# Kernel tuning notes

Measured on AMD Instinct MI355X. Metric: run time of the kernel, lower is better.

The kernel has to match this reference:

```python
import jax, jax.numpy as jnp
import numpy as np

S, B_BOX, N_CLASS = 7, 2, 20
L_COORD, L_NOOBJ = 5.0, 0.5
BATCH = 4096
C = 5 * B_BOX + N_CLASS  # 30


def setup_inputs() -> dict:
    key = jax.random.key(0)
    k1, k2, k3, k4 = jax.random.split(key, 4)
    # coords/w/h/classes strictly positive (sqrt is applied to raw values)
    y = jax.random.uniform(k1, (BATCH, S, S, C), minval=0.05, maxval=0.95, dtype=jnp.float32)
    # confidence channels must be exactly 0/1 (mask tests == 1)
    conf0 = jax.random.bernoulli(k3, 0.3, (BATCH, S, S)).astype(jnp.float32)
    conf1 = jax.random.bernoulli(k4, 0.3, (BATCH, S, S)).astype(jnp.float32)
    y = y.at[..., 0].set(conf0).at[..., 5].set(conf1)
    y_h = jax.random.uniform(k2, (BATCH, S, S, C), minval=0.05, maxval=0.95, dtype=jnp.float32)
    return {"y": y, "y_h": y_h}


def _loss(y, y_h):
    b_sz = y.shape[0]
    conf_idx = np.arange(B_BOX) * 5  # [0, 5]
    y_conf = y[..., conf_idx]        # [B,S,S,b]
    yh_conf = y_h[..., conf_idx]
    mf = (y_conf == 1.0).astype(y.dtype)  # obj mask per box, constant wrt grads
    dconf = (y_conf - yh_conf) ** 2
    loss_obj = jnp.sum(dconf * mf)
    loss_noobj = jnp.sum(dconf * (1.0 - mf))

    loss_coord = jnp.zeros((), y.dtype)
    loss_prob = jnp.zeros((), y.dtype)
    for k in range(B_BOX):  # static small loop over boxes
        mk = mf[..., k]  # [B,S,S]
        base = 5 * k
        dxy = (y[..., base + 1] - y_h[..., base + 1]) ** 2 \
            + (y[..., base + 2] - y_h[..., base + 2]) ** 2
        dwh = (jnp.sqrt(y[..., base + 3]) - jnp.sqrt(y_h[..., base + 3])) ** 2 \
            + (jnp.sqrt(y[..., base + 4]) - jnp.sqrt(y_h[..., base + 4])) ** 2
        loss_coord = loss_coord + jnp.sum((dxy + dwh) * mk)

        # prob term: slice from k*5+5 to end (faithful to original, for k=0 this
        # includes box-2's 5 entries), softmax over the masked batch dimension.
        tail = y[..., base + 5:]
        tail_h = y_h[..., base + 5:]
        mkb = mk[..., None]  # [B,S,S,1]
        neg = jnp.where(mkb > 0, tail_h, -jnp.inf)
        m = jnp.max(neg, axis=0)                       # [S,S,Ct]
        m_safe = jnp.where(jnp.isfinite(m), m, 0.0)    # guard empty columns
        p = jnp.exp(tail_h - m_safe) * mkb
        denom = jnp.sum(p, axis=0)
        sm = p / jnp.where(denom > 0, denom, 1.0)
        loss_prob = loss_prob + jnp.sum((tail - sm) ** 2 * mkb)

    loss = loss_obj + L_NOOBJ * loss_noobj + L_COORD * loss_coord + loss_prob
    return loss / b_sz


def reference(y, y_h):
    return _loss(y, y_h)
```

## Files before the change

kernel.cpp:

```cpp
#include <hip/hip_runtime.h>
#include <math.h>

#define CC 30
#define NBATCH 4096
#define NIJ 49
#define NPAIR 1225
#define PSTR 7352
#define F4TOT (PSTR / 4)
#define THREADS 512
#define SLABF4 1470
#define SLABF  5880


__global__ __launch_bounds__(THREADS)
void yolo_main(const float* __restrict__ y, const float* __restrict__ yh,
               float* __restrict__ scal, float* __restrict__ parts, int nwg)
{
    __shared__ __align__(16) float tY[2][SLABF];
    __shared__ __align__(16) float tH[2][SLABF];
    __shared__ float scr[4][8];

    const int tid = threadIdx.x;
    const int wg  = blockIdx.x;
    const int bpw = NBATCH / nwg;
    const int nslab = bpw >> 2;

    const int i0 = tid, i1 = tid + 512;
    const int i2r = tid + 1024;
    const int i2  = (i2r < SLABF4) ? i2r : (SLABF4 - 1);
    const bool w2 = (i2r < SLABF4);

    int  ijv[3], cv[3], pr[3];
    bool val[3];
    #pragma unroll
    for (int i = 0; i < 3; i++) {
        int p = tid + i * THREADS;
        val[i] = (p < NPAIR);
        pr[i]  = p;
        int pp = val[i] ? p : 0;
        ijv[i] = pp / 25;
        cv[i]  = 5 + pp % 25;
    }

    float D0[3] = {0,0,0}, B0[3] = {0,0,0}, C0[3] = {0,0,0};
    float D1[3] = {0,0,0}, B1[3] = {0,0,0}, C1[3] = {0,0,0};
    float obj = 0.f, noobj = 0.f, coord = 0.f, tt = 0.f;

    const float4* Yg = (const float4*)y;
    const float4* Hg = (const float4*)yh;

    {
        const size_t f4 = (size_t)((wg * bpw) >> 2) * SLABF4;
        float4 a0 = Yg[f4+i0], a1 = Yg[f4+i1], a2 = Yg[f4+i2];
        float4 b0 = Hg[f4+i0], b1 = Hg[f4+i1], b2 = Hg[f4+i2];
        float4* dY = (float4*)tY[0];
        float4* dH = (float4*)tH[0];
        dY[i0] = a0; dY[i1] = a1; if (w2) dY[i2] = a2;
        dH[i0] = b0; dH[i1] = b1; if (w2) dH[i2] = b2;
    }
    __syncthreads();

    for (int s = 0; s < nslab; s++) {
        const float* cy = tY[s & 1];
        const float* ch = tH[s & 1];
        const bool pf = (s + 1 < nslab);
        float4 ry0, ry1, ry2, rh0, rh1, rh2;
        if (pf) {
            const size_t nf4 = (size_t)((wg * bpw + (s+1)*4) >> 2) * SLABF4;
            ry0 = Yg[nf4+i0]; ry1 = Yg[nf4+i1]; ry2 = Yg[nf4+i2];
            rh0 = Hg[nf4+i0]; rh1 = Hg[nf4+i1]; rh2 = Hg[nf4+i2];
        }

        if (tid < 4 * NIJ) {
            const int base = tid * CC;
            float y0 = cy[base],     h0 = ch[base];
            float y5 = cy[base + 5], h5 = ch[base + 5];
            float d0 = y0 - h0; d0 *= d0;
            float d5 = y5 - h5; d5 *= d5;
            const bool m0 = (y0 == 1.0f), m1 = (y5 == 1.0f);
            obj   += (m0 ? d0 : 0.f) + (m1 ? d5 : 0.f);
            noobj += (m0 ? 0.f : d0) + (m1 ? 0.f : d5);
            if (m0) {
                float a  = cy[base + 1] - ch[base + 1];
                float b2 = cy[base + 2] - ch[base + 2];
                float c1 = sqrtf(cy[base + 3]) - sqrtf(ch[base + 3]);
                float c2 = sqrtf(cy[base + 4]) - sqrtf(ch[base + 4]);
                coord += a * a + b2 * b2 + c1 * c1 + c2 * c2;
            }
            if (m1) {
                float a  = cy[base + 6] - ch[base + 6];
                float b2 = cy[base + 7] - ch[base + 7];
                float c1 = sqrtf(cy[base + 8]) - sqrtf(ch[base + 8]);
                float c2 = sqrtf(cy[base + 9]) - sqrtf(ch[base + 9]);
                coord += a * a + b2 * b2 + c1 * c1 + c2 * c2;
            }
        }

        #pragma unroll
        for (int b = 0; b < 4; b++) {
            #pragma unroll
            for (int i = 0; i < 3; i++) {
                if (!val[i]) continue;
                const int cb = b * 1470 + ijv[i] * CC;
                const float w0 = (cy[cb] == 1.0f) ? 1.f : 0.f;
                const float wk = (cv[i] >= 10 && cy[cb + 5] == 1.0f) ? 1.f : 0.f;
                const float t  = cy[cb + cv[i]];
                const float th = ch[cb + cv[i]];
                const float e  = __expf(th);
                const float te = t * e, ee = e * e, t2 = t * t;
                D0[i] = fmaf(e,  w0, D0[i]);
                B0[i] = fmaf(te, w0, B0[i]);
                C0[i] = fmaf(ee, w0, C0[i]);
                D1[i] = fmaf(e,  wk, D1[i]);
                B1[i] = fmaf(te, wk, B1[i]);
                C1[i] = fmaf(ee, wk, C1[i]);
                tt = fmaf(t2, w0 + wk, tt);
            }
        }

        if (pf) {
            float4* dY = (float4*)tY[(s + 1) & 1];
            float4* dH = (float4*)tH[(s + 1) & 1];
            dY[i0] = ry0; dY[i1] = ry1; if (w2) dY[i2] = ry2;
            dH[i0] = rh0; dH[i1] = rh1; if (w2) dH[i2] = rh2;
        }
        __syncthreads();
    }

    float* pp = parts + (size_t)wg * PSTR;
    #pragma unroll
    for (int i = 0; i < 3; i++) {
        if (!val[i]) continue;
        const int p = pr[i];
        pp[p]            = D0[i];
        pp[NPAIR + p]    = B0[i];
        pp[2*NPAIR + p]  = C0[i];
        pp[3*NPAIR + p]  = D1[i];
        pp[4*NPAIR + p]  = B1[i];
        pp[5*NPAIR + p]  = C1[i];
    }

    const int lane = tid & 63, wv = tid >> 6;
    #pragma unroll
    for (int off = 32; off > 0; off >>= 1) {
        obj   += __shfl_down(obj,   off);
        noobj += __shfl_down(noobj, off);
        coord += __shfl_down(coord, off);
        tt    += __shfl_down(tt,    off);
    }
    if (lane == 0) { scr[0][wv] = obj; scr[1][wv] = noobj; scr[2][wv] = coord; scr[3][wv] = tt; }
    __syncthreads();
    if (tid < 4) {
        float sacc = 0.f;
        #pragma unroll
        for (int w = 0; w < THREADS / 64; w++) sacc += scr[tid][w];
        scal[wg * 4 + tid] = sacc;
    }
}

__global__ __launch_bounds__(512)
void yolo_reduce(const float* __restrict__ parts, float* __restrict__ parts2, int nwg)
{
    const int lane = threadIdx.x & 63;
    const int sub  = threadIdx.x >> 6;
    const int f4i  = blockIdx.x * 64 + lane;
    const int cy   = blockIdx.y;
    const int wpc  = nwg >> 3;
    const int wps  = wpc >> 3;

    float4 s = make_float4(0.f, 0.f, 0.f, 0.f);
    if (f4i < F4TOT) {
        const float* q = parts + (size_t)(cy * wpc + sub * wps) * PSTR + f4i * 4;
        for (int w = 0; w < wps; ++w) {
            float4 a = *(const float4*)q;
            s.x += a.x; s.y += a.y; s.z += a.z; s.w += a.w;
            q += PSTR;
        }
    }
    __shared__ float4 sred[8][64];
    sred[sub][lane] = s;
    __syncthreads();
    if (threadIdx.x < 64 && f4i < F4TOT) {
        float4 t = sred[0][lane];
        #pragma unroll
        for (int c = 1; c < 8; c++) {
            float4 a = sred[c][lane];
            t.x += a.x; t.y += a.y; t.z += a.z; t.w += a.w;
        }
        *(float4*)(parts2 + (size_t)cy * PSTR + f4i * 4) = t;
    }
}

__global__ __launch_bounds__(1024)
void yolo_final(const float* __restrict__ parts2, const float* __restrict__ scal,
                float* __restrict__ out, int nwg)
{
    float v = 0.f;

    for (int s = threadIdx.x; s < NPAIR; s += 1024) {
        const int cidx = s % 25;
        float D0 = 0, B0 = 0, C0 = 0, D1 = 0, B1 = 0, C1 = 0;
        #pragma unroll
        for (int c = 0; c < 8; c++) {
            const float* t = parts2 + (size_t)c * PSTR;
            D0 += t[s];           B0 += t[NPAIR + s];   C0 += t[2*NPAIR + s];
            D1 += t[3*NPAIR + s]; B1 += t[4*NPAIR + s]; C1 += t[5*NPAIR + s];
        }
        if (D0 > 0.f) v += C0 / (D0 * D0) - 2.f * B0 / D0;
        if (cidx >= 5 && D1 > 0.f) v += C1 / (D1 * D1) - 2.f * B1 / D1;
    }

    const float4* s4 = (const float4*)scal;
    for (int w = threadIdx.x; w < nwg; w += 1024) {
        float4 a = s4[w];
        v += a.x + 0.5f * a.y + 5.0f * a.z + a.w;
    }

    __shared__ float sred[16];
    #pragma unroll
    for (int off = 32; off > 0; off >>= 1) v += __shfl_down(v, off);
    const int lane = threadIdx.x & 63, wv = threadIdx.x >> 6;
    if (lane == 0) sred[wv] = v;
    __syncthreads();
    if (threadIdx.x == 0) {
        float tot = 0.f;
        #pragma unroll
        for (int w = 0; w < 16; w++) tot += sred[w];
        out[0] = tot / (float)NBATCH;
    }
}

extern "C" void kernel_launch(void* const* d_in, const int* in_sizes, int n_in,
                              void* d_out, int out_size, void* d_ws, size_t ws_size,
                              hipStream_t stream)
{
    const float* y  = (const float*)d_in[0];
    const float* yh = (const float*)d_in[1];
    float* out    = (float*)d_out;
    float* scal   = (float*)d_ws;
    float* parts2 = (float*)((char*)d_ws + 8192);
    float* parts  = (float*)((char*)d_ws + 243456);

    const size_t per_wg = (size_t)PSTR * sizeof(float);
    int nwg;
    if      (ws_size >= 243456 + 256 * per_wg) nwg = 256;
    else if (ws_size >= 243456 + 128 * per_wg) nwg = 128;
    else                                       nwg = 64;

    yolo_main<<<nwg, THREADS, 0, stream>>>(y, yh, scal, parts, nwg);
    dim3 g2((F4TOT + 63) / 64, 8);
    yolo_reduce<<<g2, 512, 0, stream>>>(parts, parts2, nwg);
    yolo_final<<<1, 1024, 0, stream>>>(parts2, scal, out, nwg);
}
```

Baseline: 27.48 us.

## Batch-load four slabs into registers before staged LDS compute

Replaces the one-slab-ahead double-buffered prefetch loop with a scheme that issues global loads for four slabs at once into registers. It then cycles them through the two LDS buffers with a barrier between each write and compute. The goal is more memory-level parallelism and fewer exposed load latencies per workgroup. It also adds a launch_bounds minimum of 2 blocks. The 24 live float4 registers raise VGPR pressure, which under that register cap could cause spills. The loop now assumes the slab count is a multiple of four.

```diff
diff --git a/kernel.cpp b/kernel.cpp
--- a/kernel.cpp
+++ b/kernel.cpp
@@ -12,7 +12,7 @@
 #define SLABF  5880
 
 
-__global__ __launch_bounds__(THREADS)
+__global__ __launch_bounds__(THREADS, 2)
 void yolo_main(const float* __restrict__ y, const float* __restrict__ yh,
                float* __restrict__ scal, float* __restrict__ parts, int nwg)
 {
@@ -48,84 +48,98 @@
 
     const float4* Yg = (const float4*)y;
     const float4* Hg = (const float4*)yh;
-
-    {
-        const size_t f4 = (size_t)((wg * bpw) >> 2) * SLABF4;
-        float4 a0 = Yg[f4+i0], a1 = Yg[f4+i1], a2 = Yg[f4+i2];
-        float4 b0 = Hg[f4+i0], b1 = Hg[f4+i1], b2 = Hg[f4+i2];
-        float4* dY = (float4*)tY[0];
-        float4* dH = (float4*)tH[0];
-        dY[i0] = a0; dY[i1] = a1; if (w2) dY[i2] = a2;
-        dH[i0] = b0; dH[i1] = b1; if (w2) dH[i2] = b2;
-    }
-    __syncthreads();
-
-    for (int s = 0; s < nslab; s++) {
-        const float* cy = tY[s & 1];
-        const float* ch = tH[s & 1];
-        const bool pf = (s + 1 < nslab);
-        float4 ry0, ry1, ry2, rh0, rh1, rh2;
-        if (pf) {
-            const size_t nf4 = (size_t)((wg * bpw + (s+1)*4) >> 2) * SLABF4;
-            ry0 = Yg[nf4+i0]; ry1 = Yg[nf4+i1]; ry2 = Yg[nf4+i2];
-            rh0 = Hg[nf4+i0]; rh1 = Hg[nf4+i1]; rh2 = Hg[nf4+i2];
-        }
-
-        if (tid < 4 * NIJ) {
-            const int base = tid * CC;
-            float y0 = cy[base],     h0 = ch[base];
-            float y5 = cy[base + 5], h5 = ch[base + 5];
-            float d0 = y0 - h0; d0 *= d0;
-            float d5 = y5 - h5; d5 *= d5;
-            const bool m0 = (y0 == 1.0f), m1 = (y5 == 1.0f);
-            obj   += (m0 ? d0 : 0.f) + (m1 ? d5 : 0.f);
-            noobj += (m0 ? 0.f : d0) + (m1 ? 0.f : d5);
-            if (m0) {
-                float a  = cy[base + 1] - ch[base + 1];
-                float b2 = cy[base + 2] - ch[base + 2];
-                float c1 = sqrtf(cy[base + 3]) - sqrtf(ch[base + 3]);
-                float c2 = sqrtf(cy[base + 4]) - sqrtf(ch[base + 4]);
-                coord += a * a + b2 * b2 + c1 * c1 + c2 * c2;
-            }
-            if (m1) {
-                float a  = cy[base + 6] - ch[base + 6];
-                float b2 = cy[base + 7] - ch[base + 7];
-                float c1 = sqrtf(cy[base + 8]) - sqrtf(ch[base + 8]);
-                float c2 = sqrtf(cy[base + 9]) - sqrtf(ch[base + 9]);
-                coord += a * a + b2 * b2 + c1 * c1 + c2 * c2;
-            }
-        }
-
-        #pragma unroll
-        for (int b = 0; b < 4; b++) {
-            #pragma unroll
-            for (int i = 0; i < 3; i++) {
-                if (!val[i]) continue;
-                const int cb = b * 1470 + ijv[i] * CC;
-                const float w0 = (cy[cb] == 1.0f) ? 1.f : 0.f;
-                const float wk = (cv[i] >= 10 && cy[cb + 5] == 1.0f) ? 1.f : 0.f;
-                const float t  = cy[cb + cv[i]];
-                const float th = ch[cb + cv[i]];
-                const float e  = __expf(th);
-                const float te = t * e, ee = e * e, t2 = t * t;
-                D0[i] = fmaf(e,  w0, D0[i]);
-                B0[i] = fmaf(te, w0, B0[i]);
-                C0[i] = fmaf(ee, w0, C0[i]);
-                D1[i] = fmaf(e,  wk, D1[i]);
-                B1[i] = fmaf(te, wk, B1[i]);
-                C1[i] = fmaf(ee, wk, C1[i]);
-                tt = fmaf(t2, w0 + wk, tt);
-            }
-        }
-
-        if (pf) {
-            float4* dY = (float4*)tY[(s + 1) & 1];
-            float4* dH = (float4*)tH[(s + 1) & 1];
-            dY[i0] = ry0; dY[i1] = ry1; if (w2) dY[i2] = ry2;
-            dH[i0] = rh0; dH[i1] = rh1; if (w2) dH[i2] = rh2;
-        }
-        __syncthreads();
-    }
+    const int sb = wg * (bpw >> 2);
+
+#define COMPUTE(BUF)                                                            \
+    {                                                                           \
+        const float* cy = tY[BUF];                                              \
+        const float* ch = tH[BUF];                                              \
+        if (tid < 4 * NIJ) {                                                    \
+            const int base = tid * CC;                                          \
+            float y0 = cy[base],     h0 = ch[base];                             \
+            float y5 = cy[base + 5], h5 = ch[base + 5];                         \
+            float d0 = y0 - h0; d0 *= d0;                                       \
+            float d5 = y5 - h5; d5 *= d5;                                       \
+            const bool m0 = (y0 == 1.0f), m1 = (y5 == 1.0f);                    \
+            obj   += (m0 ? d0 : 0.f) + (m1 ? d5 : 0.f);                         \
+            noobj += (m0 ? 0.f : d0) + (m1 ? 0.f : d5);                         \
+            if (m0) {                                                           \
+                float a  = cy[base + 1] - ch[base + 1];                         \
+                float b2 = cy[base + 2] - ch[base + 2];                         \
+                float c1 = sqrtf(cy[base + 3]) - sqrtf(ch[base + 3]);           \
+                float c2 = sqrtf(cy[base + 4]) - sqrtf(ch[base + 4]);           \
+                coord += a * a + b2 * b2 + c1 * c1 + c2 * c2;                   \
+            }                                                                   \
+            if (m1) {                                                           \
+                float a  = cy[base + 6] - ch[base + 6];                         \
+                float b2 = cy[base + 7] - ch[base + 7];                         \
+                float c1 = sqrtf(cy[base + 8]) - sqrtf(ch[base + 8]);           \
+                float c2 = sqrtf(cy[base + 9]) - sqrtf(ch[base + 9]);           \
+                coord += a * a + b2 * b2 + c1 * c1 + c2 * c2;                   \
+            }                                                                   \
+        }                                                                       \
+        _Pragma("unroll")                                                       \
+        for (int b = 0; b < 4; b++) {                                           \
+            _Pragma("unroll")                                                   \
+            for (int i = 0; i < 3; i++) {                                       \
+                if (!val[i]) continue;                                          \
+                const int cb = b * 1470 + ijv[i] * CC;                          \
+                const float w0 = (cy[cb] == 1.0f) ? 1.f : 0.f;                  \
+                const float wk = (cv[i] >= 10 && cy[cb + 5] == 1.0f) ? 1.f : 0.f;\
+                const float t  = cy[cb + cv[i]];                                \
+                const float th = ch[cb + cv[i]];                                \
+                const float e  = __expf(th);                                    \
+                const float te = t * e, ee = e * e, t2 = t * t;                 \
+                D0[i] = fmaf(e,  w0, D0[i]);                                    \
+                B0[i] = fmaf(te, w0, B0[i]);                                    \
+                C0[i] = fmaf(ee, w0, C0[i]);                                    \
+                D1[i] = fmaf(e,  wk, D1[i]);                                    \
+                B1[i] = fmaf(te, wk, B1[i]);                                    \
+                C1[i] = fmaf(ee, wk, C1[i]);                                    \
+                tt = fmaf(t2, w0 + wk, tt);                                     \
+            }                                                                   \
+        }                                                                       \
+    }
+
+#define WRITE(BUF, Y0, Y1, Y2, H0, H1, H2)                                      \
+    {                                                                           \
+        float4* dY = (float4*)tY[BUF];                                          \
+        float4* dH = (float4*)tH[BUF];                                          \
+        dY[i0] = Y0; dY[i1] = Y1; if (w2) dY[i2] = Y2;                          \
+        dH[i0] = H0; dH[i1] = H1; if (w2) dH[i2] = H2;                          \
+    }
+
+    for (int ss = 0; ss < nslab; ss += 4) {
+        const size_t b0 = (size_t)(sb + ss) * SLABF4;
+        const size_t b1 = b0 + SLABF4, b2 = b0 + 2 * SLABF4, b3 = b0 + 3 * SLABF4;
+        float4 ya0 = Yg[b0+i0], ya1 = Yg[b0+i1], ya2 = Yg[b0+i2];
+        float4 ha0 = Hg[b0+i0], ha1 = Hg[b0+i1], ha2 = Hg[b0+i2];
+        float4 yb0 = Yg[b1+i0], yb1 = Yg[b1+i1], yb2 = Yg[b1+i2];
+        float4 hb0 = Hg[b1+i0], hb1 = Hg[b1+i1], hb2 = Hg[b1+i2];
+        float4 yc0 = Yg[b2+i0], yc1 = Yg[b2+i1], yc2 = Yg[b2+i2];
+        float4 hc0 = Hg[b2+i0], hc1 = Hg[b2+i1], hc2 = Hg[b2+i2];
+        float4 yd0 = Yg[b3+i0], yd1 = Yg[b3+i1], yd2 = Yg[b3+i2];
+        float4 hd0 = Hg[b3+i0], hd1 = Hg[b3+i1], hd2 = Hg[b3+i2];
+
+        WRITE(0, ya0, ya1, ya2, ha0, ha1, ha2);
+        __syncthreads();
+
+        COMPUTE(0);
+        WRITE(1, yb0, yb1, yb2, hb0, hb1, hb2);
+        __syncthreads();
+
+        COMPUTE(1);
+        WRITE(0, yc0, yc1, yc2, hc0, hc1, hc2);
+        __syncthreads();
+
+        COMPUTE(0);
+        WRITE(1, yd0, yd1, yd2, hd0, hd1, hd2);
+        __syncthreads();
+
+        COMPUTE(1);
+    }
+#undef COMPUTE
+#undef WRITE
 
     float* pp = parts + (size_t)wg * PSTR;
     #pragma unroll
```

Result: slower. 32.55 us (+18.5%).

## Stream inputs straight to LDS with a 4-slot ring and prefetch depth two

Applied to the files above, without the earlier changes.

The main kernel previously staged each 4-batch slab through registers and double-buffered it in LDS. It now splits the work into 2-batch units and fetches them with global_load_lds (direct global-to-LDS DMA) into a 4-slot ring, keeping two units in flight. Waves 0-3 load y and waves 4-7 load y_h. Synchronisation uses explicit s_waitcnt vmcnt counts plus one barrier per unit. The goal is more memory-level parallelism and fewer register and VGPR round trips. The cost is reliance on hand-tuned waitcnt counts and more LDS use.

```diff
diff --git a/kernel.cpp b/kernel.cpp
--- a/kernel.cpp
+++ b/kernel.cpp
@@ -8,27 +8,32 @@
 #define PSTR 7352
 #define F4TOT (PSTR / 4)
 #define THREADS 512
-#define SLABF4 1470
-#define SLABF  5880
-
+#define UNITF4 768
+#define UNITF  3072
+
+
+__device__ __forceinline__ void gload_lds16(const void* g, void* l) {
+    __builtin_amdgcn_global_load_lds(
+        (const __attribute__((address_space(1))) void*)g,
+        (__attribute__((address_space(3))) void*)l, 16, 0, 0);
+}
 
 __global__ __launch_bounds__(THREADS)
 void yolo_main(const float* __restrict__ y, const float* __restrict__ yh,
                float* __restrict__ scal, float* __restrict__ parts, int nwg)
 {
-    __shared__ __align__(16) float tY[2][SLABF];
-    __shared__ __align__(16) float tH[2][SLABF];
+    __shared__ __align__(16) float ldsY[4][UNITF];
+    __shared__ __align__(16) float ldsH[4][UNITF];
     __shared__ float scr[4][8];
 
-    const int tid = threadIdx.x;
-    const int wg  = blockIdx.x;
-    const int bpw = NBATCH / nwg;
-    const int nslab = bpw >> 2;
-
-    const int i0 = tid, i1 = tid + 512;
-    const int i2r = tid + 1024;
-    const int i2  = (i2r < SLABF4) ? i2r : (SLABF4 - 1);
-    const bool w2 = (i2r < SLABF4);
+    const int tid  = threadIdx.x;
+    const int wg   = blockIdx.x;
+    const int bpw  = NBATCH / nwg;
+    const int nunit = bpw >> 1;
+    const int wid  = tid >> 6;
+    const int lane = tid & 63;
+    const int wsub = wid & 3;
+    const bool isY = (wid < 4);
 
     int  ijv[3], cv[3], pr[3];
     bool val[3];
@@ -46,32 +51,38 @@
     float D1[3] = {0,0,0}, B1[3] = {0,0,0}, C1[3] = {0,0,0};
     float obj = 0.f, noobj = 0.f, coord = 0.f, tt = 0.f;
 
-    const float4* Yg = (const float4*)y;
-    const float4* Hg = (const float4*)yh;
-
-    {
-        const size_t f4 = (size_t)((wg * bpw) >> 2) * SLABF4;
-        float4 a0 = Yg[f4+i0], a1 = Yg[f4+i1], a2 = Yg[f4+i2];
-        float4 b0 = Hg[f4+i0], b1 = Hg[f4+i1], b2 = Hg[f4+i2];
-        float4* dY = (float4*)tY[0];
-        float4* dH = (float4*)tH[0];
-        dY[i0] = a0; dY[i1] = a1; if (w2) dY[i2] = a2;
-        dH[i0] = b0; dH[i1] = b1; if (w2) dH[i2] = b2;
-    }
-    __syncthreads();
-
-    for (int s = 0; s < nslab; s++) {
-        const float* cy = tY[s & 1];
-        const float* ch = tH[s & 1];
-        const bool pf = (s + 1 < nslab);
-        float4 ry0, ry1, ry2, rh0, rh1, rh2;
-        if (pf) {
-            const size_t nf4 = (size_t)((wg * bpw + (s+1)*4) >> 2) * SLABF4;
-            ry0 = Yg[nf4+i0]; ry1 = Yg[nf4+i1]; ry2 = Yg[nf4+i2];
-            rh0 = Hg[nf4+i0]; rh1 = Hg[nf4+i1]; rh2 = Hg[nf4+i2];
-        }
-
-        if (tid < 4 * NIJ) {
+    const float4* gsrc = isY ? (const float4*)y : (const float4*)yh;
+
+#define ISSUE(uu) {                                                             \
+        const int    rs_  = (uu) & 3;                                           \
+        const size_t bas_ = 735ull * ((size_t)wg * (bpw >> 1) + (uu));          \
+        float* ld_ = isY ? ldsY[rs_] : ldsH[rs_];                               \
+        _Pragma("unroll")                                                       \
+        for (int r_ = 0; r_ < 3; r_++) {                                        \
+            const int idx_ = r_ * 256 + wsub * 64 + lane;                       \
+            const int src_ = idx_ > 734 ? 734 : idx_;                           \
+            gload_lds16(gsrc + bas_ + src_, ld_ + (size_t)idx_ * 4);            \
+        } }
+
+    ISSUE(0);
+    ISSUE(1);
+
+    for (int u = 0; u < nunit; u++) {
+        if (u < nunit - 2) {
+            ISSUE(u + 2);
+            asm volatile("s_waitcnt vmcnt(6)" ::: "memory");
+        } else if (u == nunit - 2) {
+            asm volatile("s_waitcnt vmcnt(3)" ::: "memory");
+        } else {
+            asm volatile("s_waitcnt vmcnt(0)" ::: "memory");
+        }
+        __builtin_amdgcn_s_barrier();
+
+        const int rs = u & 3;
+        const float* cy = ldsY[rs];
+        const float* ch = ldsH[rs];
+
+        if (tid < 2 * NIJ) {
             const int base = tid * CC;
             float y0 = cy[base],     h0 = ch[base];
             float y5 = cy[base + 5], h5 = ch[base + 5];
@@ -97,7 +108,7 @@
         }
 
         #pragma unroll
-        for (int b = 0; b < 4; b++) {
+        for (int b = 0; b < 2; b++) {
             #pragma unroll
             for (int i = 0; i < 3; i++) {
                 if (!val[i]) continue;
@@ -117,15 +128,8 @@
                 tt = fmaf(t2, w0 + wk, tt);
             }
         }
-
-        if (pf) {
-            float4* dY = (float4*)tY[(s + 1) & 1];
-            float4* dH = (float4*)tH[(s + 1) & 1];
-            dY[i0] = ry0; dY[i1] = ry1; if (w2) dY[i2] = ry2;
-            dH[i0] = rh0; dH[i1] = rh1; if (w2) dH[i2] = rh2;
-        }
-        __syncthreads();
-    }
+    }
+#undef ISSUE
 
     float* pp = parts + (size_t)wg * PSTR;
     #pragma unroll
@@ -140,7 +144,7 @@
         pp[5*NPAIR + p]  = C1[i];
     }
 
-    const int lane = tid & 63, wv = tid >> 6;
+    const int wv = wid;
     #pragma unroll
     for (int off = 32; off > 0; off >>= 1) {
         obj   += __shfl_down(obj,   off);
```

Measured after the change: 29.14 us. +6.0%, slower.

## Replace partial-sum buffers and reduce kernel with fixed-point 64-bit atomics

Applied to the files above, without the earlier changes.

Each workgroup now converts its per-pair softmax partials and scalar terms to 2^40-scaled integers and atomically adds them into one shared u64 table. The table is zeroed by a small kernel, and the final kernel decodes it in double precision. This removes the per-workgroup partial buffer writes and the separate reduce kernel, and skips the unused D1/B1/C1 entries. In exchange it adds roughly 7k-9k 64-bit atomics per workgroup with contention across 256 blocks, a zeroing launch, and a risk of precision loss or overflow from the fixed-point encoding.

```diff
diff --git a/kernel.cpp b/kernel.cpp
--- a/kernel.cpp
+++ b/kernel.cpp
@@ -5,16 +5,26 @@
 #define NBATCH 4096
 #define NIJ 49
 #define NPAIR 1225
-#define PSTR 7352
-#define F4TOT (PSTR / 4)
 #define THREADS 512
 #define SLABF4 1470
 #define SLABF  5880
-
+#define NTBL   (6 * NPAIR + 4)
+#define SCALE  1099511627776.0
+#define INVSCALE (1.0 / 1099511627776.0)
+
+typedef unsigned long long u64;
+
+
+__global__ __launch_bounds__(512)
+void yolo_zero(u64* __restrict__ tbl)
+{
+    const int i = blockIdx.x * 512 + threadIdx.x;
+    if (i < NTBL) tbl[i] = 0ull;
+}
 
 __global__ __launch_bounds__(THREADS)
 void yolo_main(const float* __restrict__ y, const float* __restrict__ yh,
-               float* __restrict__ scal, float* __restrict__ parts, int nwg)
+               u64* __restrict__ tbl, int nwg)
 {
     __shared__ __align__(16) float tY[2][SLABF];
     __shared__ __align__(16) float tH[2][SLABF];
@@ -127,17 +137,18 @@
         __syncthreads();
     }
 
-    float* pp = parts + (size_t)wg * PSTR;
     #pragma unroll
     for (int i = 0; i < 3; i++) {
         if (!val[i]) continue;
         const int p = pr[i];
-        pp[p]            = D0[i];
-        pp[NPAIR + p]    = B0[i];
-        pp[2*NPAIR + p]  = C0[i];
-        pp[3*NPAIR + p]  = D1[i];
-        pp[4*NPAIR + p]  = B1[i];
-        pp[5*NPAIR + p]  = C1[i];
+        atomicAdd(&tbl[p],             (u64)((double)D0[i] * SCALE));
+        atomicAdd(&tbl[NPAIR + p],     (u64)((double)B0[i] * SCALE));
+        atomicAdd(&tbl[2*NPAIR + p],   (u64)((double)C0[i] * SCALE));
+        if (cv[i] >= 10) {
+            atomicAdd(&tbl[3*NPAIR + p], (u64)((double)D1[i] * SCALE));
+            atomicAdd(&tbl[4*NPAIR + p], (u64)((double)B1[i] * SCALE));
+            atomicAdd(&tbl[5*NPAIR + p], (u64)((double)C1[i] * SCALE));
+        }
     }
 
     const int lane = tid & 63, wv = tid >> 6;
@@ -154,79 +165,45 @@
         float sacc = 0.f;
         #pragma unroll
         for (int w = 0; w < THREADS / 64; w++) sacc += scr[tid][w];
-        scal[wg * 4 + tid] = sacc;
-    }
-}
-
-__global__ __launch_bounds__(512)
-void yolo_reduce(const float* __restrict__ parts, float* __restrict__ parts2, int nwg)
-{
-    const int lane = threadIdx.x & 63;
-    const int sub  = threadIdx.x >> 6;
-    const int f4i  = blockIdx.x * 64 + lane;
-    const int cy   = blockIdx.y;
-    const int wpc  = nwg >> 3;
-    const int wps  = wpc >> 3;
-
-    float4 s = make_float4(0.f, 0.f, 0.f, 0.f);
-    if (f4i < F4TOT) {
-        const float* q = parts + (size_t)(cy * wpc + sub * wps) * PSTR + f4i * 4;
-        for (int w = 0; w < wps; ++w) {
-            float4 a = *(const float4*)q;
-            s.x += a.x; s.y += a.y; s.z += a.z; s.w += a.w;
-            q += PSTR;
-        }
-    }
-    __shared__ float4 sred[8][64];
-    sred[sub][lane] = s;
-    __syncthreads();
-    if (threadIdx.x < 64 && f4i < F4TOT) {
-        float4 t = sred[0][lane];
-        #pragma unroll
-        for (int c = 1; c < 8; c++) {
-            float4 a = sred[c][lane];
-            t.x += a.x; t.y += a.y; t.z += a.z; t.w += a.w;
-        }
-        *(float4*)(parts2 + (size_t)cy * PSTR + f4i * 4) = t;
+        atomicAdd(&tbl[6*NPAIR + tid], (u64)((double)sacc * SCALE));
     }
 }
 
 __global__ __launch_bounds__(1024)
-void yolo_final(const float* __restrict__ parts2, const float* __restrict__ scal,
-                float* __restrict__ out, int nwg)
-{
-    float v = 0.f;
+void yolo_final(const u64* __restrict__ tbl, float* __restrict__ out)
+{
+    double v = 0.0;
 
     for (int s = threadIdx.x; s < NPAIR; s += 1024) {
         const int cidx = s % 25;
-        float D0 = 0, B0 = 0, C0 = 0, D1 = 0, B1 = 0, C1 = 0;
-        #pragma unroll
-        for (int c = 0; c < 8; c++) {
-            const float* t = parts2 + (size_t)c * PSTR;
-            D0 += t[s];           B0 += t[NPAIR + s];   C0 += t[2*NPAIR + s];
-            D1 += t[3*NPAIR + s]; B1 += t[4*NPAIR + s]; C1 += t[5*NPAIR + s];
-        }
-        if (D0 > 0.f) v += C0 / (D0 * D0) - 2.f * B0 / D0;
-        if (cidx >= 5 && D1 > 0.f) v += C1 / (D1 * D1) - 2.f * B1 / D1;
-    }
-
-    const float4* s4 = (const float4*)scal;
-    for (int w = threadIdx.x; w < nwg; w += 1024) {
-        float4 a = s4[w];
-        v += a.x + 0.5f * a.y + 5.0f * a.z + a.w;
-    }
-
-    __shared__ float sred[16];
+        double D0 = (double)tbl[s]           * INVSCALE;
+        double B0 = (double)tbl[NPAIR + s]   * INVSCALE;
+        double C0 = (double)tbl[2*NPAIR + s] * INVSCALE;
+        if (D0 > 0.0) v += C0 / (D0 * D0) - 2.0 * B0 / D0;
+        if (cidx >= 5) {
+            double D1 = (double)tbl[3*NPAIR + s] * INVSCALE;
+            double B1 = (double)tbl[4*NPAIR + s] * INVSCALE;
+            double C1 = (double)tbl[5*NPAIR + s] * INVSCALE;
+            if (D1 > 0.0) v += C1 / (D1 * D1) - 2.0 * B1 / D1;
+        }
+    }
+
+    __shared__ double sred[16];
     #pragma unroll
     for (int off = 32; off > 0; off >>= 1) v += __shfl_down(v, off);
     const int lane = threadIdx.x & 63, wv = threadIdx.x >> 6;
     if (lane == 0) sred[wv] = v;
     __syncthreads();
     if (threadIdx.x == 0) {
-        float tot = 0.f;
+        double tot = 0.0;
         #pragma unroll
         for (int w = 0; w < 16; w++) tot += sred[w];
-        out[0] = tot / (float)NBATCH;
+        double obj   = (double)tbl[6*NPAIR + 0] * INVSCALE;
+        double noobj = (double)tbl[6*NPAIR + 1] * INVSCALE;
+        double coord = (double)tbl[6*NPAIR + 2] * INVSCALE;
+        double tts   = (double)tbl[6*NPAIR + 3] * INVSCALE;
+        double loss = obj + 0.5 * noobj + 5.0 * coord + tts + tot;
+        out[0] = (float)(loss / (double)NBATCH);
     }
 }
 
@@ -236,19 +213,11 @@
 {
     const float* y  = (const float*)d_in[0];
     const float* yh = (const float*)d_in[1];
-    float* out    = (float*)d_out;
-    float* scal   = (float*)d_ws;
-    float* parts2 = (float*)((char*)d_ws + 8192);
-    float* parts  = (float*)((char*)d_ws + 243456);
-
-    const size_t per_wg = (size_t)PSTR * sizeof(float);
-    int nwg;
-    if      (ws_size >= 243456 + 256 * per_wg) nwg = 256;
-    else if (ws_size >= 243456 + 128 * per_wg) nwg = 128;
-    else                                       nwg = 64;
-
-    yolo_main<<<nwg, THREADS, 0, stream>>>(y, yh, scal, parts, nwg);
-    dim3 g2((F4TOT + 63) / 64, 8);
-    yolo_reduce<<<g2, 512, 0, stream>>>(parts, parts2, nwg);
-    yolo_final<<<1, 1024, 0, stream>>>(parts2, scal, out, nwg);
-}
+    float* out = (float*)d_out;
+    u64*   tbl = (u64*)d_ws;
+
+    const int nwg = 256;
+    yolo_zero<<<(NTBL + 511) / 512, 512, 0, stream>>>(tbl);
+    yolo_main<<<nwg, THREADS, 0, stream>>>(y, yh, tbl, nwg);
+    yolo_final<<<1, 1024, 0, stream>>>(tbl, out);
+}
```

Measured after the change: 45.03 us. 63.9% more time.
